# Optimization experiments

Measured on AMD Instinct MI355X. Metric: run time of the kernel, lower is better.

The kernel has to match this reference:

```python
import jax, jax.numpy as jnp
import numpy as np

N, K, D = 32768, 8192, 512
COMMITMENT_COST = 0.25

def setup_inputs() -> dict:
    key = jax.random.key(0)
    k1, k2 = jax.random.split(key)
    z_e = jax.random.normal(k1, (N, D), dtype=jnp.float32)
    # codebook init: uniform(-1/K, 1/K) as in nn.init.uniform_
    codebook = jax.random.uniform(k2, (K, D), dtype=jnp.float32, minval=-1.0 / K, maxval=1.0 / K)
    return {"z_e": z_e, "codebook": codebook}

def reference(z_e, codebook):
    # squared L2 distances: ||z||^2 + ||e||^2 - 2 z.e^T  -> (N, K)
    z_sq = jnp.sum(z_e * z_e, axis=1, keepdims=True)          # (N, 1)
    e_sq = jnp.sum(codebook * codebook, axis=1)[None, :]       # (1, K)
    distances = z_sq + e_sq - 2.0 * jnp.matmul(z_e, codebook.T)
    indices = jnp.argmin(distances, axis=1)                    # (N,)
    z_q = codebook[indices]                                    # (N, D)
    z_q_st = z_e + jax.lax.stop_gradient(z_q - z_e)
    codebook_loss = jnp.mean((z_q - jax.lax.stop_gradient(z_e)) ** 2)
    commitment_loss = COMMITMENT_COST * jnp.mean((z_e - jax.lax.stop_gradient(z_q)) ** 2)
    return (z_q_st, indices, codebook_loss, commitment_loss)
```

## Files before the change

### kernel.cpp

```cpp
#include <hip/hip_runtime.h>

#define NROWS 32768
#define KCB   8192
#define DDIM  512
#define MT 64
#define KT 128
#define DC 32
#define CAP 32
#define MARGIN 4.88e-4f

typedef short bf16x8 __attribute__((ext_vector_type(8)));
typedef float f32x4  __attribute__((ext_vector_type(4)));

static __device__ __forceinline__ unsigned short f2bf(float f) {
  unsigned u = __float_as_uint(f);
  return (unsigned short)((u + 0x7fffu + ((u >> 16) & 1u)) >> 16);
}

static __device__ __forceinline__ float exact_dot(const float* __restrict__ zp,
                                                  const float* __restrict__ ep) {
  float a = 0.f;
#pragma unroll 8
  for (int d = 0; d < DDIM; d += 4) {
    float4 zv = *(const float4*)(zp + d);
    float4 ev = *(const float4*)(ep + d);
    a = fmaf(zv.x, ev.x, a);
    a = fmaf(zv.y, ev.y, a);
    a = fmaf(zv.z, ev.z, a);
    a = fmaf(zv.w, ev.w, a);
  }
  return a;
}

__global__ __launch_bounds__(256) void sq_pairwise_kernel(
    const float* __restrict__ z, const float* __restrict__ cb,
    float* __restrict__ zsq, float* __restrict__ esq)
{
#pragma clang fp contract(off)
  int gtid = blockIdx.x * 256 + threadIdx.x;
  int row  = gtid >> 5;
  int l    = threadIdx.x & 31;
  if (row >= NROWS + KCB) return;
  const float* src = (row < NROWS) ? (z + (size_t)row * DDIM)
                                   : (cb + (size_t)(row - NROWS) * DDIM);
  int blk = l >> 3, j = l & 7;
  const float* p = src + blk * 128 + j;
  float acc = 0.0f;
#pragma unroll
  for (int t = 0; t < 16; ++t) {
    float v = p[8 * t];
    float q = v * v;
    acc = acc + q;
  }
  float s = acc + __shfl_xor(acc, 1);
  s = s + __shfl_xor(s, 2);
  s = s + __shfl_xor(s, 4);
  float u = s + __shfl_xor(s, 8);
  u = u + __shfl_xor(u, 16);
  if (l == 0) {
    if (row < NROWS) zsq[row] = u;
    else             esq[row - NROWS] = u;
  }
}

__global__ __launch_bounds__(256) void cvt_cb_kernel(
    const float* __restrict__ cb, unsigned short* __restrict__ cbb)
{
  int t = blockIdx.x * 256 + threadIdx.x;
  const float4* src = (const float4*)(cb + (size_t)t * 8);
  float4 f0 = src[0], f1 = src[1];
  ushort4 o0, o1;
  o0.x = f2bf(f0.x); o0.y = f2bf(f0.y); o0.z = f2bf(f0.z); o0.w = f2bf(f0.w);
  o1.x = f2bf(f1.x); o1.y = f2bf(f1.y); o1.z = f2bf(f1.z); o1.w = f2bf(f1.w);
  *(ushort4*)(cbb + (size_t)t * 8) = o0;
  *(ushort4*)(cbb + (size_t)t * 8 + 4) = o1;
}

__global__ __launch_bounds__(256) void vq_mfma_kernel(
    const float* __restrict__ z, const float* __restrict__ cb,
    const unsigned short* __restrict__ cbb,
    const float* __restrict__ zsq, const float* __restrict__ esq,
    float* __restrict__ out_zq, float* __restrict__ out_idx,
    double* __restrict__ loss_acc)
{
  __shared__ char BsRaw[2][16384];
  __shared__ int cnt[MT];
  __shared__ int lists[MT][CAP];
  __shared__ unsigned long long bestpk[MT];
  __shared__ double red_sh[4];

  const int tid = threadIdx.x;
  const int l   = tid & 63;
  const int w   = tid >> 6;
  const int row0  = blockIdx.x * MT;
  const int wrow0 = row0 + w * 16;

  for (int i = tid; i < MT; i += 256) { cnt[i] = 0; bestpk[i] = ~0ull; }

  bf16x8 afrag[16];
  {
    const float* zrow = z + (size_t)(wrow0 + (l & 15)) * DDIM + ((l >> 4) << 3);
#pragma unroll
    for (int c = 0; c < 16; ++c) {
      float4 f0 = *(const float4*)(zrow + c * 32);
      float4 f1 = *(const float4*)(zrow + c * 32 + 4);
      bf16x8 a;
      a[0] = (short)f2bf(f0.x); a[1] = (short)f2bf(f0.y);
      a[2] = (short)f2bf(f0.z); a[3] = (short)f2bf(f0.w);
      a[4] = (short)f2bf(f1.x); a[5] = (short)f2bf(f1.y);
      a[6] = (short)f2bf(f1.z); a[7] = (short)f2bf(f1.w);
      afrag[c] = a;
    }
  }

  float zs_r[4];
#pragma unroll
  for (int r = 0; r < 4; ++r) zs_r[r] = zsq[wrow0 + ((l >> 4) << 2) + r];

  float m_r[4] = {3.4e38f, 3.4e38f, 3.4e38f, 3.4e38f};

  f32x4 acc[8];
#pragma unroll
  for (int nf = 0; nf < 8; ++nf) acc[nf] = (f32x4)0.f;

#define STAGE(BUF, CI)                                                          \
  {                                                                             \
    int k0s = ((CI) >> 3) * KT;                                                 \
    int d0b = ((CI) & 7) * 128;                                                 \
    _Pragma("unroll")                                                           \
    for (int i = 0; i < 4; ++i) {                                               \
      int slot = i * 256 + tid;                                                 \
      int brow = slot >> 3;                                                     \
      int dgrp = slot & 7;                                                      \
      int4 v = *(const int4*)((const char*)cbb + (size_t)(k0s + brow) * 1024    \
                              + d0b + dgrp * 16);                               \
      int wb = brow * 128 + ((dgrp * 16) ^ ((brow & 7) << 4));                  \
      *(int4*)(&BsRaw[BUF][wb]) = v;                                            \
    }                                                                           \
  }

  __syncthreads();
  STAGE(0, 0)

  const int rbase = (l & 15) * 128;
  const int dsw   = ((l >> 4) << 4);
  const int lxor  = (l & 7) << 4;

  for (int ci = 0; ci < 512; ++ci) {
    __syncthreads();
    if (ci + 1 < 512) STAGE((ci + 1) & 1, ci + 1)
    const char* bufp = &BsRaw[ci & 1][0];
    const int ai = (ci & 7) << 1;
#pragma unroll
    for (int nf = 0; nf < 8; ++nf) {
#pragma unroll
      for (int sub = 0; sub < 2; ++sub) {
        int off = nf * 2048 + rbase + ((sub * 64 + dsw) ^ lxor);
        bf16x8 bfrag = *(const bf16x8*)(bufp + off);
        acc[nf] = __builtin_amdgcn_mfma_f32_16x16x32_bf16(afrag[ai + sub], bfrag,
                                                          acc[nf], 0, 0, 0);
      }
    }

    if ((ci & 7) == 7) {
      int k0 = (ci >> 3) * KT;
      float eq[8];
#pragma unroll
      for (int nf = 0; nf < 8; ++nf) eq[nf] = esq[k0 + (nf << 4) + (l & 15)];
#pragma unroll
      for (int nf = 0; nf < 8; ++nf)
#pragma unroll
        for (int r = 0; r < 4; ++r)
          acc[nf][r] = (zs_r[r] + eq[nf]) - 2.0f * acc[nf][r];

      float rm[4];
#pragma unroll
      for (int r = 0; r < 4; ++r) {
        float m01 = fminf(fminf(acc[0][r], acc[1][r]), fminf(acc[2][r], acc[3][r]));
        float m23 = fminf(fminf(acc[4][r], acc[5][r]), fminf(acc[6][r], acc[7][r]));
        float v = fminf(m01, m23);
        v = fminf(v, __shfl_xor(v, 1));
        v = fminf(v, __shfl_xor(v, 2));
        v = fminf(v, __shfl_xor(v, 4));
        v = fminf(v, __shfl_xor(v, 8));
        rm[r] = v;
        m_r[r] = fminf(m_r[r], v);
      }
      bool anyq = false;
#pragma unroll
      for (int nf = 0; nf < 8; ++nf)
#pragma unroll
        for (int r = 0; r < 4; ++r)
          anyq |= (acc[nf][r] <= m_r[r] + MARGIN);
      if (__any(anyq)) {
#pragma unroll
        for (int nf = 0; nf < 8; ++nf)
#pragma unroll
          for (int r = 0; r < 4; ++r)
            if (acc[nf][r] <= m_r[r] + MARGIN) {
              int rowloc = (w << 4) + ((l >> 4) << 2) + r;
              int pos = atomicAdd(&cnt[rowloc], 1);
              if (pos < CAP) lists[rowloc][pos] = k0 + (nf << 4) + (l & 15);
            }
      }
#pragma unroll
      for (int nf = 0; nf < 8; ++nf) acc[nf] = (f32x4)0.f;
    }
  }
  __syncthreads();

  {
    int r = tid >> 2;
    int grow = row0 + r;
    int c = cnt[r] < CAP ? cnt[r] : CAP;
    const float* zp = z + (size_t)grow * DDIM;
    float zsv = zsq[grow];
    for (int s = tid & 3; s < c; s += 4) {
      int k = lists[r][s];
      float dot = exact_dot(zp, cb + (size_t)k * DDIM);
      float dist = (zsv + esq[k]) - 2.0f * dot;
      unsigned long long pk =
          ((unsigned long long)__float_as_uint(dist) << 32) | (unsigned)k;
      atomicMin(&bestpk[r], pk);
    }
  }
  __syncthreads();

  for (int r2 = 0; r2 < MT; ++r2) {
    if (cnt[r2] > CAP) {
      int grow = row0 + r2;
      const float* zp = z + (size_t)grow * DDIM;
      float zsv = zsq[grow];
      for (int k = tid; k < KCB; k += 256) {
        float dot = exact_dot(zp, cb + (size_t)k * DDIM);
        float dist = (zsv + esq[k]) - 2.0f * dot;
        unsigned long long pk =
            ((unsigned long long)__float_as_uint(dist) << 32) | (unsigned)k;
        atomicMin(&bestpk[r2], pk);
      }
    }
  }
  __syncthreads();

  if (tid < MT) out_idx[row0 + tid] = (float)(unsigned)(bestpk[tid] & 0xffffffffu);

  double lsum = 0.0;
  for (int t4 = tid; t4 < MT * (DDIM / 4); t4 += 256) {
    int r   = t4 >> 7;
    int c4  = t4 & 127;
    int grow = row0 + r;
    int kidx = (int)(unsigned)(bestpk[r] & 0xffffffffu);
    float4 zv  = *(const float4*)(z  + (size_t)grow * DDIM + (c4 << 2));
    float4 cv4 = *(const float4*)(cb + (size_t)kidx * DDIM + (c4 << 2));
    float t0 = cv4.x - zv.x;
    float t1 = cv4.y - zv.y;
    float t2 = cv4.z - zv.z;
    float t3 = cv4.w - zv.w;
    float4 o;
    o.x = zv.x + t0; o.y = zv.y + t1; o.z = zv.z + t2; o.w = zv.w + t3;
    *(float4*)(out_zq + (size_t)grow * DDIM + (c4 << 2)) = o;
    lsum += (double)t0 * t0 + (double)t1 * t1 + (double)t2 * t2 + (double)t3 * t3;
  }
#pragma unroll
  for (int off = 32; off >= 1; off >>= 1) lsum += __shfl_xor(lsum, off);
  if ((tid & 63) == 0) red_sh[tid >> 6] = lsum;
  __syncthreads();
  if (tid == 0) {
    double s = (red_sh[0] + red_sh[1]) + (red_sh[2] + red_sh[3]);
    atomicAdd(loss_acc, s);
  }
}

__global__ __launch_bounds__(256) void vq_main_kernel(
    const float* __restrict__ z, const float* __restrict__ cb,
    const float* __restrict__ zsq, const float* __restrict__ esq,
    float* __restrict__ out_zq, float* __restrict__ out_idx,
    double* __restrict__ loss_acc)
{
  __shared__ float As[DC][68];
  __shared__ float Bs[DC][140];
  __shared__ int   idx_sh[MT];
  __shared__ double red_sh[4];

  const int tid  = threadIdx.x;
  const int row0 = blockIdx.x * MT;
  const int ty = tid >> 4;
  const int tx = tid & 15;

  const int arow = tid >> 2;
  const int adof = (tid & 3) << 3;
  const int brow = tid >> 1;
  const int bdof = (tid & 1) << 4;
  const int bcolw = brow + ((brow >> 5) << 2);
  const int bcolr = (tx << 3) + ((tx >> 2) << 2);

  float zs[4];
#pragma unroll
  for (int i = 0; i < 4; ++i) zs[i] = zsq[row0 + (ty << 2) + i];

  float bvbest[4]; int bibest[4];
#pragma unroll
  for (int i = 0; i < 4; ++i) { bvbest[i] = 3.402823466e38f; bibest[i] = 0x7fffffff; }

  for (int k0 = 0; k0 < KCB; k0 += KT) {
    float acc[4][8];
#pragma unroll
    for (int i = 0; i < 4; ++i)
#pragma unroll
      for (int jj = 0; jj < 8; ++jj) acc[i][jj] = 0.0f;

    for (int d0 = 0; d0 < DDIM; d0 += DC) {
      const float4* ag = (const float4*)(z + (size_t)(row0 + arow) * DDIM + d0 + adof);
      float4 a0 = ag[0];
      float4 a1 = ag[1];
      const float4* bg = (const float4*)(cb + (size_t)(k0 + brow) * DDIM + d0 + bdof);
      float4 b0 = bg[0], b1 = bg[1], b2 = bg[2], b3 = bg[3];
      __syncthreads();
      As[adof + 0][arow] = a0.x; As[adof + 1][arow] = a0.y;
      As[adof + 2][arow] = a0.z; As[adof + 3][arow] = a0.w;
      As[adof + 4][arow] = a1.x; As[adof + 5][arow] = a1.y;
      As[adof + 6][arow] = a1.z; As[adof + 7][arow] = a1.w;
      Bs[bdof +  0][bcolw] = b0.x; Bs[bdof +  1][bcolw] = b0.y;
      Bs[bdof +  2][bcolw] = b0.z; Bs[bdof +  3][bcolw] = b0.w;
      Bs[bdof +  4][bcolw] = b1.x; Bs[bdof +  5][bcolw] = b1.y;
      Bs[bdof +  6][bcolw] = b1.z; Bs[bdof +  7][bcolw] = b1.w;
      Bs[bdof +  8][bcolw] = b2.x; Bs[bdof +  9][bcolw] = b2.y;
      Bs[bdof + 10][bcolw] = b2.z; Bs[bdof + 11][bcolw] = b2.w;
      Bs[bdof + 12][bcolw] = b3.x; Bs[bdof + 13][bcolw] = b3.y;
      Bs[bdof + 14][bcolw] = b3.z; Bs[bdof + 15][bcolw] = b3.w;
      __syncthreads();
#pragma unroll 8
      for (int dc = 0; dc < DC; ++dc) {
        float4 a4 = *(const float4*)&As[dc][ty << 2];
        float4 p0 = *(const float4*)&Bs[dc][bcolr];
        float4 p1 = *(const float4*)&Bs[dc][bcolr + 4];
        float av[4] = {a4.x, a4.y, a4.z, a4.w};
        float bw[8] = {p0.x, p0.y, p0.z, p0.w, p1.x, p1.y, p1.z, p1.w};
#pragma unroll
        for (int i = 0; i < 4; ++i)
#pragma unroll
          for (int jj = 0; jj < 8; ++jj)
            acc[i][jj] += av[i] * bw[jj];
      }
    }

    float ek[8];
#pragma unroll
    for (int jj = 0; jj < 8; ++jj) ek[jj] = esq[k0 + (tx << 3) + jj];
#pragma unroll
    for (int i = 0; i < 4; ++i) {
      float cv = 3.402823466e38f; int ci = 0x7fffffff;
#pragma unroll
      for (int jj = 0; jj < 8; ++jj) {
        int k = k0 + (tx << 3) + jj;
        float t1 = zs[i] + ek[jj];
        float dist = t1 - 2.0f * acc[i][jj];
        if (dist < cv || (dist == cv && k < ci)) { cv = dist; ci = k; }
      }
#pragma unroll
      for (int off = 1; off < 16; off <<= 1) {
        float ov = __shfl_xor(cv, off);
        int   oi = __shfl_xor(ci, off);
        if (ov < cv || (ov == cv && oi < ci)) { cv = ov; ci = oi; }
      }
      if (cv < bvbest[i] || (cv == bvbest[i] && ci < bibest[i])) {
        bvbest[i] = cv; bibest[i] = ci;
      }
    }
  }

  if (tx == 0) {
#pragma unroll
    for (int i = 0; i < 4; ++i) idx_sh[(ty << 2) + i] = bibest[i];
  }
  __syncthreads();

  double lsum = 0.0;
  for (int t4 = tid; t4 < MT * (DDIM / 4); t4 += 256) {
    int r   = t4 >> 7;
    int c4  = t4 & 127;
    int grow = row0 + r;
    int kidx = idx_sh[r];
    float4 zv  = *(const float4*)(z  + (size_t)grow * DDIM + (c4 << 2));
    float4 cv4 = *(const float4*)(cb + (size_t)kidx * DDIM + (c4 << 2));
    float t0 = cv4.x - zv.x;
    float t1 = cv4.y - zv.y;
    float t2 = cv4.z - zv.z;
    float t3 = cv4.w - zv.w;
    float4 o;
    o.x = zv.x + t0; o.y = zv.y + t1; o.z = zv.z + t2; o.w = zv.w + t3;
    *(float4*)(out_zq + (size_t)grow * DDIM + (c4 << 2)) = o;
    lsum += (double)t0 * t0 + (double)t1 * t1 + (double)t2 * t2 + (double)t3 * t3;
  }
#pragma unroll
  for (int off = 32; off >= 1; off >>= 1) lsum += __shfl_xor(lsum, off);
  if ((tid & 63) == 0) red_sh[tid >> 6] = lsum;
  __syncthreads();
  if (tid == 0) {
    double s = (red_sh[0] + red_sh[1]) + (red_sh[2] + red_sh[3]);
    atomicAdd(loss_acc, s);
  }

  if (tid < MT) out_idx[row0 + tid] = (float)idx_sh[tid];
}

__global__ void vq_finalize_kernel(const double* __restrict__ loss_acc,
                                   float* __restrict__ out_sc)
{
  double m = loss_acc[0] * (1.0 / 16777216.0);
  float mf = (float)m;
  out_sc[0] = mf;
  out_sc[1] = 0.25f * mf;
}

extern "C" void kernel_launch(void* const* d_in, const int* in_sizes, int n_in,
                              void* d_out, int out_size, void* d_ws, size_t ws_size,
                              hipStream_t stream)
{
  const float* z  = (const float*)d_in[0];
  const float* cb = (const float*)d_in[1];
  float* out     = (float*)d_out;
  float* out_zq  = out;
  float* out_idx = out + (size_t)NROWS * DDIM;
  float* out_sc  = out_idx + NROWS;

  double* acc = (double*)d_ws;
  float* zsq = (float*)((char*)d_ws + 256);
  float* esq = zsq + NROWS;
  unsigned short* cbb = (unsigned short*)((char*)d_ws + (1 << 20));

  hipMemsetAsync(d_ws, 0, 8, stream);
  hipLaunchKernelGGL(sq_pairwise_kernel, dim3((NROWS + KCB) / 8), dim3(256), 0, stream,
                     z, cb, zsq, esq);
  if (ws_size >= (size_t)10 * 1024 * 1024) {
    hipLaunchKernelGGL(cvt_cb_kernel, dim3(KCB * DDIM / 8 / 256), dim3(256), 0, stream,
                       cb, cbb);
    hipLaunchKernelGGL(vq_mfma_kernel, dim3(NROWS / MT), dim3(256), 0, stream,
                       z, cb, cbb, zsq, esq, out_zq, out_idx, acc);
  } else {
    hipLaunchKernelGGL(vq_main_kernel, dim3(NROWS / MT), dim3(256), 0, stream,
                       z, cb, zsq, esq, out_zq, out_idx, acc);
  }
  hipLaunchKernelGGL(vq_finalize_kernel, dim3(1), dim3(1), 0, stream, acc, out_sc);
}
```

Measured before the change: 849.5 us.

## Double rows per wave in MFMA VQ kernel and stage codebook via direct-to-LDS loads

Each wave now computes 32 rows instead of 16, holding two A-fragment sets and two accumulator sets, so every codebook B fragment read from shared memory feeds two MFMAs. This halves codebook staging traffic per output row. Codebook staging now uses global_load_lds DMA with the swizzle applied on the global address side, which removes the register round trip. The changes raise register pressure (launch bounds set to one block per CU) and halve the grid to 256 blocks, which may underfill the device. The tail rescoring now uses two threads per row instead of four.

```diff
diff --git a/kernel.cpp b/kernel.cpp
--- a/kernel.cpp
+++ b/kernel.cpp
@@ -3,9 +3,8 @@
 #define NROWS 32768
 #define KCB   8192
 #define DDIM  512
-#define MT 64
+#define MT 128
 #define KT 128
-#define DC 32
 #define CAP 32
 #define MARGIN 4.88e-4f
 
@@ -15,6 +14,12 @@
 static __device__ __forceinline__ unsigned short f2bf(float f) {
   unsigned u = __float_as_uint(f);
   return (unsigned short)((u + 0x7fffu + ((u >> 16) & 1u)) >> 16);
+}
+
+static __device__ __forceinline__ void gload_lds16(const void* g, void* l) {
+  __builtin_amdgcn_global_load_lds(
+      (const __attribute__((address_space(1))) unsigned int*)g,
+      (__attribute__((address_space(3))) unsigned int*)l, 16, 0, 0);
 }
 
 static __device__ __forceinline__ float exact_dot(const float* __restrict__ zp,
@@ -76,14 +81,14 @@
   *(ushort4*)(cbb + (size_t)t * 8 + 4) = o1;
 }
 
-__global__ __launch_bounds__(256) void vq_mfma_kernel(
+__global__ __launch_bounds__(256, 1) void vq_mfma_kernel(
     const float* __restrict__ z, const float* __restrict__ cb,
     const unsigned short* __restrict__ cbb,
     const float* __restrict__ zsq, const float* __restrict__ esq,
     float* __restrict__ out_zq, float* __restrict__ out_idx,
     double* __restrict__ loss_acc)
 {
-  __shared__ char BsRaw[2][16384];
+  __shared__ alignas(16) char BsRaw[2][16384];
   __shared__ int cnt[MT];
   __shared__ int lists[MT][CAP];
   __shared__ unsigned long long bestpk[MT];
@@ -93,54 +98,65 @@
   const int l   = tid & 63;
   const int w   = tid >> 6;
   const int row0  = blockIdx.x * MT;
-  const int wrow0 = row0 + w * 16;
+  const int wrow0 = row0 + w * 32;
 
   for (int i = tid; i < MT; i += 256) { cnt[i] = 0; bestpk[i] = ~0ull; }
 
-  bf16x8 afrag[16];
+  bf16x8 afragL[16], afragH[16];
   {
-    const float* zrow = z + (size_t)(wrow0 + (l & 15)) * DDIM + ((l >> 4) << 3);
+    const float* zrowL = z + (size_t)(wrow0 + (l & 15)) * DDIM + ((l >> 4) << 3);
+    const float* zrowH = zrowL + 16 * DDIM;
 #pragma unroll
     for (int c = 0; c < 16; ++c) {
-      float4 f0 = *(const float4*)(zrow + c * 32);
-      float4 f1 = *(const float4*)(zrow + c * 32 + 4);
+      float4 f0 = *(const float4*)(zrowL + c * 32);
+      float4 f1 = *(const float4*)(zrowL + c * 32 + 4);
       bf16x8 a;
       a[0] = (short)f2bf(f0.x); a[1] = (short)f2bf(f0.y);
       a[2] = (short)f2bf(f0.z); a[3] = (short)f2bf(f0.w);
       a[4] = (short)f2bf(f1.x); a[5] = (short)f2bf(f1.y);
       a[6] = (short)f2bf(f1.z); a[7] = (short)f2bf(f1.w);
-      afrag[c] = a;
-    }
-  }
-
-  float zs_r[4];
-#pragma unroll
-  for (int r = 0; r < 4; ++r) zs_r[r] = zsq[wrow0 + ((l >> 4) << 2) + r];
-
-  float m_r[4] = {3.4e38f, 3.4e38f, 3.4e38f, 3.4e38f};
-
-  f32x4 acc[8];
-#pragma unroll
-  for (int nf = 0; nf < 8; ++nf) acc[nf] = (f32x4)0.f;
-
-#define STAGE(BUF, CI)                                                          \
+      afragL[c] = a;
+      f0 = *(const float4*)(zrowH + c * 32);
+      f1 = *(const float4*)(zrowH + c * 32 + 4);
+      a[0] = (short)f2bf(f0.x); a[1] = (short)f2bf(f0.y);
+      a[2] = (short)f2bf(f0.z); a[3] = (short)f2bf(f0.w);
+      a[4] = (short)f2bf(f1.x); a[5] = (short)f2bf(f1.y);
+      a[6] = (short)f2bf(f1.z); a[7] = (short)f2bf(f1.w);
+      afragH[c] = a;
+    }
+  }
+
+  float zs_r[8];
+#pragma unroll
+  for (int r = 0; r < 4; ++r) {
+    zs_r[r]     = zsq[wrow0 + ((l >> 4) << 2) + r];
+    zs_r[4 + r] = zsq[wrow0 + 16 + ((l >> 4) << 2) + r];
+  }
+
+  float m_r[8];
+#pragma unroll
+  for (int r = 0; r < 8; ++r) m_r[r] = 3.4e38f;
+
+  f32x4 accL[8], accH[8];
+#pragma unroll
+  for (int nf = 0; nf < 8; ++nf) { accL[nf] = (f32x4)0.f; accH[nf] = (f32x4)0.f; }
+
+  const int gswz = (((l & 7) ^ (l >> 3)) << 4);
+#define STAGE_DMA(BUF, CI)                                                      \
   {                                                                             \
     int k0s = ((CI) >> 3) * KT;                                                 \
     int d0b = ((CI) & 7) * 128;                                                 \
+    const char* gbase = (const char*)cbb + (size_t)k0s * 1024 + d0b + gswz;     \
     _Pragma("unroll")                                                           \
-    for (int i = 0; i < 4; ++i) {                                               \
-      int slot = i * 256 + tid;                                                 \
-      int brow = slot >> 3;                                                     \
-      int dgrp = slot & 7;                                                      \
-      int4 v = *(const int4*)((const char*)cbb + (size_t)(k0s + brow) * 1024    \
-                              + d0b + dgrp * 16);                               \
-      int wb = brow * 128 + ((dgrp * 16) ^ ((brow & 7) << 4));                  \
-      *(int4*)(&BsRaw[BUF][wb]) = v;                                            \
+    for (int c = 0; c < 4; ++c) {                                               \
+      int seg = (w << 2) + c;                                                   \
+      gload_lds16(gbase + (size_t)((seg << 3) + (l >> 3)) * 1024,               \
+                  &BsRaw[BUF][seg << 10]);                                      \
     }                                                                           \
   }
 
   __syncthreads();
-  STAGE(0, 0)
+  STAGE_DMA(0, 0)
 
   const int rbase = (l & 15) * 128;
   const int dsw   = ((l >> 4) << 4);
@@ -148,7 +164,7 @@
 
   for (int ci = 0; ci < 512; ++ci) {
     __syncthreads();
-    if (ci + 1 < 512) STAGE((ci + 1) & 1, ci + 1)
+    if (ci + 1 < 512) STAGE_DMA((ci + 1) & 1, ci + 1)
     const char* bufp = &BsRaw[ci & 1][0];
     const int ai = (ci & 7) << 1;
 #pragma unroll
@@ -157,8 +173,10 @@
       for (int sub = 0; sub < 2; ++sub) {
         int off = nf * 2048 + rbase + ((sub * 64 + dsw) ^ lxor);
         bf16x8 bfrag = *(const bf16x8*)(bufp + off);
-        acc[nf] = __builtin_amdgcn_mfma_f32_16x16x32_bf16(afrag[ai + sub], bfrag,
-                                                          acc[nf], 0, 0, 0);
+        accL[nf] = __builtin_amdgcn_mfma_f32_16x16x32_bf16(afragL[ai + sub], bfrag,
+                                                           accL[nf], 0, 0, 0);
+        accH[nf] = __builtin_amdgcn_mfma_f32_16x16x32_bf16(afragH[ai + sub], bfrag,
+                                                           accH[nf], 0, 0, 0);
       }
     }
 
@@ -170,52 +188,64 @@
 #pragma unroll
       for (int nf = 0; nf < 8; ++nf)
 #pragma unroll
-        for (int r = 0; r < 4; ++r)
-          acc[nf][r] = (zs_r[r] + eq[nf]) - 2.0f * acc[nf][r];
-
-      float rm[4];
+        for (int r = 0; r < 4; ++r) {
+          accL[nf][r] = (zs_r[r] + eq[nf]) - 2.0f * accL[nf][r];
+          accH[nf][r] = (zs_r[4 + r] + eq[nf]) - 2.0f * accH[nf][r];
+        }
 #pragma unroll
       for (int r = 0; r < 4; ++r) {
-        float m01 = fminf(fminf(acc[0][r], acc[1][r]), fminf(acc[2][r], acc[3][r]));
-        float m23 = fminf(fminf(acc[4][r], acc[5][r]), fminf(acc[6][r], acc[7][r]));
-        float v = fminf(m01, m23);
-        v = fminf(v, __shfl_xor(v, 1));
-        v = fminf(v, __shfl_xor(v, 2));
-        v = fminf(v, __shfl_xor(v, 4));
-        v = fminf(v, __shfl_xor(v, 8));
-        rm[r] = v;
-        m_r[r] = fminf(m_r[r], v);
+        float vL = fminf(fminf(fminf(accL[0][r], accL[1][r]), fminf(accL[2][r], accL[3][r])),
+                         fminf(fminf(accL[4][r], accL[5][r]), fminf(accL[6][r], accL[7][r])));
+        float vH = fminf(fminf(fminf(accH[0][r], accH[1][r]), fminf(accH[2][r], accH[3][r])),
+                         fminf(fminf(accH[4][r], accH[5][r]), fminf(accH[6][r], accH[7][r])));
+        vL = fminf(vL, __shfl_xor(vL, 1));
+        vL = fminf(vL, __shfl_xor(vL, 2));
+        vL = fminf(vL, __shfl_xor(vL, 4));
+        vL = fminf(vL, __shfl_xor(vL, 8));
+        vH = fminf(vH, __shfl_xor(vH, 1));
+        vH = fminf(vH, __shfl_xor(vH, 2));
+        vH = fminf(vH, __shfl_xor(vH, 4));
+        vH = fminf(vH, __shfl_xor(vH, 8));
+        m_r[r]     = fminf(m_r[r], vL);
+        m_r[4 + r] = fminf(m_r[4 + r], vH);
       }
       bool anyq = false;
 #pragma unroll
       for (int nf = 0; nf < 8; ++nf)
 #pragma unroll
-        for (int r = 0; r < 4; ++r)
-          anyq |= (acc[nf][r] <= m_r[r] + MARGIN);
+        for (int r = 0; r < 4; ++r) {
+          anyq |= (accL[nf][r] <= m_r[r] + MARGIN);
+          anyq |= (accH[nf][r] <= m_r[4 + r] + MARGIN);
+        }
       if (__any(anyq)) {
+        int rowbase = (w << 5) + ((l >> 4) << 2);
 #pragma unroll
         for (int nf = 0; nf < 8; ++nf)
 #pragma unroll
-          for (int r = 0; r < 4; ++r)
-            if (acc[nf][r] <= m_r[r] + MARGIN) {
-              int rowloc = (w << 4) + ((l >> 4) << 2) + r;
-              int pos = atomicAdd(&cnt[rowloc], 1);
-              if (pos < CAP) lists[rowloc][pos] = k0 + (nf << 4) + (l & 15);
+          for (int r = 0; r < 4; ++r) {
+            if (accL[nf][r] <= m_r[r] + MARGIN) {
+              int pos = atomicAdd(&cnt[rowbase + r], 1);
+              if (pos < CAP) lists[rowbase + r][pos] = k0 + (nf << 4) + (l & 15);
             }
-      }
-#pragma unroll
-      for (int nf = 0; nf < 8; ++nf) acc[nf] = (f32x4)0.f;
+            if (accH[nf][r] <= m_r[4 + r] + MARGIN) {
+              int pos = atomicAdd(&cnt[rowbase + 16 + r], 1);
+              if (pos < CAP) lists[rowbase + 16 + r][pos] = k0 + (nf << 4) + (l & 15);
+            }
+          }
+      }
+#pragma unroll
+      for (int nf = 0; nf < 8; ++nf) { accL[nf] = (f32x4)0.f; accH[nf] = (f32x4)0.f; }
     }
   }
   __syncthreads();
 
   {
-    int r = tid >> 2;
+    int r = tid >> 1;
     int grow = row0 + r;
     int c = cnt[r] < CAP ? cnt[r] : CAP;
     const float* zp = z + (size_t)grow * DDIM;
     float zsv = zsq[grow];
-    for (int s = tid & 3; s < c; s += 4) {
+    for (int s = tid & 1; s < c; s += 2) {
       int k = lists[r][s];
       float dot = exact_dot(zp, cb + (size_t)k * DDIM);
       float dist = (zsv + esq[k]) - 2.0f * dot;
@@ -271,19 +301,21 @@
   }
 }
 
+#define FMT 64
+#define FDC 32
 __global__ __launch_bounds__(256) void vq_main_kernel(
     const float* __restrict__ z, const float* __restrict__ cb,
     const float* __restrict__ zsq, const float* __restrict__ esq,
     float* __restrict__ out_zq, float* __restrict__ out_idx,
     double* __restrict__ loss_acc)
 {
-  __shared__ float As[DC][68];
-  __shared__ float Bs[DC][140];
-  __shared__ int   idx_sh[MT];
+  __shared__ float As[FDC][68];
+  __shared__ float Bs[FDC][140];
+  __shared__ int   idx_sh[FMT];
   __shared__ double red_sh[4];
 
   const int tid  = threadIdx.x;
-  const int row0 = blockIdx.x * MT;
+  const int row0 = blockIdx.x * FMT;
   const int ty = tid >> 4;
   const int tx = tid & 15;
 
@@ -309,7 +341,7 @@
 #pragma unroll
       for (int jj = 0; jj < 8; ++jj) acc[i][jj] = 0.0f;
 
-    for (int d0 = 0; d0 < DDIM; d0 += DC) {
+    for (int d0 = 0; d0 < DDIM; d0 += FDC) {
       const float4* ag = (const float4*)(z + (size_t)(row0 + arow) * DDIM + d0 + adof);
       float4 a0 = ag[0];
       float4 a1 = ag[1];
@@ -330,7 +362,7 @@
       Bs[bdof + 14][bcolw] = b3.z; Bs[bdof + 15][bcolw] = b3.w;
       __syncthreads();
 #pragma unroll 8
-      for (int dc = 0; dc < DC; ++dc) {
+      for (int dc = 0; dc < FDC; ++dc) {
         float4 a4 = *(const float4*)&As[dc][ty << 2];
         float4 p0 = *(const float4*)&Bs[dc][bcolr];
         float4 p1 = *(const float4*)&Bs[dc][bcolr + 4];
@@ -376,7 +408,7 @@
   __syncthreads();
 
   double lsum = 0.0;
-  for (int t4 = tid; t4 < MT * (DDIM / 4); t4 += 256) {
+  for (int t4 = tid; t4 < FMT * (DDIM / 4); t4 += 256) {
     int r   = t4 >> 7;
     int c4  = t4 & 127;
     int grow = row0 + r;
@@ -401,7 +433,7 @@
     atomicAdd(loss_acc, s);
   }
 
-  if (tid < MT) out_idx[row0 + tid] = (float)idx_sh[tid];
+  if (tid < FMT) out_idx[row0 + tid] = (float)idx_sh[tid];
 }
 
 __global__ void vq_finalize_kernel(const double* __restrict__ loss_acc,
@@ -438,7 +470,7 @@
     hipLaunchKernelGGL(vq_mfma_kernel, dim3(NROWS / MT), dim3(256), 0, stream,
                        z, cb, cbb, zsq, esq, out_zq, out_idx, acc);
   } else {
-    hipLaunchKernelGGL(vq_main_kernel, dim3(NROWS / MT), dim3(256), 0, stream,
+    hipLaunchKernelGGL(vq_main_kernel, dim3(NROWS / 64), dim3(256), 0, stream,
                        z, cb, zsq, esq, out_zq, out_idx, acc);
   }
   hipLaunchKernelGGL(vq_finalize_kernel, dim3(1), dim3(1), 0, stream, acc, out_sc);
```

Measured after the change: 1.216 ms. +43.2%, slower.
